# Optimization experiments

Hardware: AMD Instinct MI355X
Metric: run time of the kernel (lower is better)

Reference implementation:

```python
import jax, jax.numpy as jnp
import numpy as np

N_NODES = 100000
N_EDGES = 1600000
D_IN = 128
D_OUT = 128


def setup_inputs() -> dict:
    key = jax.random.key(0)
    k1, k2, k3, k4, k5 = jax.random.split(key, 5)
    x = jax.random.normal(k1, (N_NODES, D_IN), dtype=jnp.float32)
    row = jax.random.randint(k2, (N_EDGES,), 0, N_NODES, dtype=jnp.int32)
    col = jax.random.randint(k3, (N_EDGES,), 0, N_NODES, dtype=jnp.int32)
    edge_weight = jax.random.uniform(k4, (N_EDGES,), dtype=jnp.float32)
    stdv = 1.0 / np.sqrt(D_OUT)
    weight = jax.random.uniform(k5, (D_IN, D_OUT), dtype=jnp.float32,
                                minval=-stdv, maxval=stdv)
    return {"x": x, "row": row, "col": col,
            "edge_weight": edge_weight, "weight": weight}


def reference(x, row, col, edge_weight, weight):
    # support = x @ W  -- dense feature transform [N, D_OUT]
    support = jnp.matmul(x, weight)
    # out = adj @ support, adj sparse COO: out[row] += w * support[col]
    messages = edge_weight[:, None] * support[col]  # [E, D_OUT]
    out = jax.ops.segment_sum(messages, row, num_segments=N_NODES)
    return out
```

## Files before the change

kernel.cpp:

```cpp
#include <hip/hip_runtime.h>

#define N_NODES 100000
#define N_EDGES 1600000
#define D 128
#define D4 32

#define BM 128
#define GEMM_BLOCKS ((N_NODES + BM - 1) / BM)
#define BUILD_BLOCKS 512
#define TOTAL_BLOCKS (BUILD_BLOCKS + GEMM_BLOCKS)
#define LDK 136

typedef __attribute__((ext_vector_type(8))) short short8;
typedef __attribute__((ext_vector_type(4))) float floatx4;

__device__ __forceinline__ unsigned short f2bf(float f) {
    unsigned int b = __float_as_uint(f);
    b += 0x7FFFu + ((b >> 16) & 1u);
    return (unsigned short)(b >> 16);
}
__device__ __forceinline__ float bf2f(unsigned short u) {
    return __uint_as_float((unsigned int)u << 16);
}

__global__ __launch_bounds__(256) void w_prep(
    const float* __restrict__ W, unsigned short* __restrict__ wt)
{
    int idx = blockIdx.x * 256 + threadIdx.x;
    int k = idx >> 7, n = idx & 127;
    wt[(size_t)n * D + k] = f2bf(W[idx]);
}

__global__ __launch_bounds__(256, 4) void mega(
    const float* __restrict__ x, const unsigned short* __restrict__ wt,
    unsigned short* __restrict__ sup,
    const int* __restrict__ row, const int* __restrict__ col,
    const float* __restrict__ ew,
    int* __restrict__ head, int4* __restrict__ entries)
{
    __shared__ unsigned short xs[BM * LDK];

    const int tid = threadIdx.x;

    if (blockIdx.x < BUILD_BLOCKS) {
        const int S = BUILD_BLOCKS * 256;
        const int par = tid & 1;
        for (int e = blockIdx.x * 256 + tid; e < N_EDGES; e += S) {
            int nx = atomicExch(&head[(row[e] << 1) | par], e);
            entries[e] = make_int4(nx, col[e], __float_as_int(ew[e]), 0);
        }
        return;
    }

    const int brow = (blockIdx.x - BUILD_BLOCKS) * BM;

    {
        const float4* xv = reinterpret_cast<const float4*>(x);
        #pragma unroll
        for (int i = 0; i < 16; ++i) {
            int idx = tid + i * 256;
            int r = idx >> 5, k4 = idx & 31;
            int gr = brow + r;
            float4 v = (gr < N_NODES) ? xv[(size_t)gr * D4 + k4]
                                      : make_float4(0.f, 0.f, 0.f, 0.f);
            ushort4 p;
            p.x = f2bf(v.x); p.y = f2bf(v.y); p.z = f2bf(v.z); p.w = f2bf(v.w);
            *reinterpret_cast<ushort4*>(&xs[r * LDK + k4 * 4]) = p;
        }
    }
    __syncthreads();

    const int wave = tid >> 6;
    const int lane = tid & 63;
    const int l15  = lane & 15;
    const int lkg  = lane >> 4;

    floatx4 acc[2][8];
    #pragma unroll
    for (int m = 0; m < 2; ++m)
        #pragma unroll
        for (int n = 0; n < 8; ++n) acc[m][n] = (floatx4){0.f, 0.f, 0.f, 0.f};

    const short8* bv = reinterpret_cast<const short8*>(wt);
    const int wrow = wave * 32;
    #pragma unroll
    for (int kk = 0; kk < 4; ++kk) {
        int kb = kk * 32 + lkg * 8;
        short8 a0 = *reinterpret_cast<const short8*>(&xs[(wrow + l15) * LDK + kb]);
        short8 a1 = *reinterpret_cast<const short8*>(&xs[(wrow + 16 + l15) * LDK + kb]);
        #pragma unroll
        for (int n = 0; n < 8; ++n) {
            short8 b = bv[(n * 16 + l15) * 16 + kk * 4 + lkg];
            acc[0][n] = __builtin_amdgcn_mfma_f32_16x16x32_bf16(a0, b, acc[0][n], 0, 0, 0);
            acc[1][n] = __builtin_amdgcn_mfma_f32_16x16x32_bf16(a1, b, acc[1][n], 0, 0, 0);
        }
    }

    const int rbase = brow + wrow + lkg * 4;
    #pragma unroll
    for (int m = 0; m < 2; ++m) {
        #pragma unroll
        for (int r = 0; r < 4; ++r) {
            int grow = rbase + m * 16 + r;
            if (grow < N_NODES) {
                #pragma unroll
                for (int n = 0; n < 8; ++n)
                    sup[(size_t)grow * D + n * 16 + l15] = f2bf(acc[m][n][r]);
            }
        }
    }
}

#define GATHER_BLOCKS (N_NODES / 16)

__global__ __launch_bounds__(256) void gather_list(
    const int* __restrict__ head, const int4* __restrict__ entries,
    const unsigned short* __restrict__ sup, float* __restrict__ out)
{
    const int half = threadIdx.x >> 5;
    const int lane = threadIdx.x & 31;
    const int nb = blockIdx.x * 16 + half * 2;

    int4 h = *reinterpret_cast<const int4*>(head + 2 * nb);
    int e0 = h.x, e1 = h.y, e2 = h.z, e3 = h.w;

    float4 A0 = {0.f, 0.f, 0.f, 0.f};
    float4 A1 = A0, A2 = A0, A3 = A0;

    while (e0 >= 0 || e1 >= 0 || e2 >= 0 || e3 >= 0) {
        int4 q0 = entries[e0 >= 0 ? e0 : 0];
        int4 q1 = entries[e1 >= 0 ? e1 : 0];
        int4 q2 = entries[e2 >= 0 ? e2 : 0];
        int4 q3 = entries[e3 >= 0 ? e3 : 0];

        ushort4 s0 = reinterpret_cast<const ushort4*>(sup + (size_t)q0.y * D)[lane];
        ushort4 s1 = reinterpret_cast<const ushort4*>(sup + (size_t)q1.y * D)[lane];
        ushort4 s2 = reinterpret_cast<const ushort4*>(sup + (size_t)q2.y * D)[lane];
        ushort4 s3 = reinterpret_cast<const ushort4*>(sup + (size_t)q3.y * D)[lane];

        float w0 = (e0 >= 0) ? __int_as_float(q0.z) : 0.f;
        float w1 = (e1 >= 0) ? __int_as_float(q1.z) : 0.f;
        float w2 = (e2 >= 0) ? __int_as_float(q2.z) : 0.f;
        float w3 = (e3 >= 0) ? __int_as_float(q3.z) : 0.f;

        A0.x = fmaf(w0, bf2f(s0.x), A0.x); A0.y = fmaf(w0, bf2f(s0.y), A0.y);
        A0.z = fmaf(w0, bf2f(s0.z), A0.z); A0.w = fmaf(w0, bf2f(s0.w), A0.w);
        A1.x = fmaf(w1, bf2f(s1.x), A1.x); A1.y = fmaf(w1, bf2f(s1.y), A1.y);
        A1.z = fmaf(w1, bf2f(s1.z), A1.z); A1.w = fmaf(w1, bf2f(s1.w), A1.w);
        A2.x = fmaf(w2, bf2f(s2.x), A2.x); A2.y = fmaf(w2, bf2f(s2.y), A2.y);
        A2.z = fmaf(w2, bf2f(s2.z), A2.z); A2.w = fmaf(w2, bf2f(s2.w), A2.w);
        A3.x = fmaf(w3, bf2f(s3.x), A3.x); A3.y = fmaf(w3, bf2f(s3.y), A3.y);
        A3.z = fmaf(w3, bf2f(s3.z), A3.z); A3.w = fmaf(w3, bf2f(s3.w), A3.w);

        e0 = (e0 >= 0) ? q0.x : -1;
        e1 = (e1 >= 0) ? q1.x : -1;
        e2 = (e2 >= 0) ? q2.x : -1;
        e3 = (e3 >= 0) ? q3.x : -1;
    }

    float4 a0, a1;
    a0.x = A0.x + A1.x; a0.y = A0.y + A1.y; a0.z = A0.z + A1.z; a0.w = A0.w + A1.w;
    a1.x = A2.x + A3.x; a1.y = A2.y + A3.y; a1.z = A2.z + A3.z; a1.w = A2.w + A3.w;

    float4* ov = reinterpret_cast<float4*>(out);
    ov[(size_t)(nb + 0) * D4 + lane] = a0;
    ov[(size_t)(nb + 1) * D4 + lane] = a1;
}

__device__ __forceinline__ void fma4(float4& a, float s, const float4& b) {
    a.x = fmaf(s, b.x, a.x);
    a.y = fmaf(s, b.y, a.y);
    a.z = fmaf(s, b.z, a.z);
    a.w = fmaf(s, b.w, a.w);
}

__global__ __launch_bounds__(256) void gemm_xw(
    const float* __restrict__ x, const float* __restrict__ W,
    unsigned short* __restrict__ sup)
{
    __shared__ float4 xs[32 * D4];
    const int tid = threadIdx.x;
    const int block_row = blockIdx.x * 32;

    const float4* xv = reinterpret_cast<const float4*>(x) + (size_t)block_row * D4;
    #pragma unroll
    for (int i = 0; i < 4; ++i) xs[tid + i * 256] = xv[tid + i * 256];
    __syncthreads();

    const int cg = tid & 31;
    const int rg = tid >> 5;
    const float4* Wv = reinterpret_cast<const float4*>(W);

    float4 acc0 = {0.f, 0.f, 0.f, 0.f};
    float4 acc1 = acc0, acc2 = acc0, acc3 = acc0;

    const int r0 = rg * 4;
    #pragma unroll 8
    for (int k4 = 0; k4 < D4; ++k4) {
        float4 xa = xs[(r0 + 0) * D4 + k4];
        float4 xb = xs[(r0 + 1) * D4 + k4];
        float4 xc = xs[(r0 + 2) * D4 + k4];
        float4 xd = xs[(r0 + 3) * D4 + k4];
        float4 w0 = Wv[(k4 * 4 + 0) * D4 + cg];
        fma4(acc0, xa.x, w0); fma4(acc1, xb.x, w0);
        fma4(acc2, xc.x, w0); fma4(acc3, xd.x, w0);
        float4 w1 = Wv[(k4 * 4 + 1) * D4 + cg];
        fma4(acc0, xa.y, w1); fma4(acc1, xb.y, w1);
        fma4(acc2, xc.y, w1); fma4(acc3, xd.y, w1);
        float4 w2 = Wv[(k4 * 4 + 2) * D4 + cg];
        fma4(acc0, xa.z, w2); fma4(acc1, xb.z, w2);
        fma4(acc2, xc.z, w2); fma4(acc3, xd.z, w2);
        float4 w3 = Wv[(k4 * 4 + 3) * D4 + cg];
        fma4(acc0, xa.w, w3); fma4(acc1, xb.w, w3);
        fma4(acc2, xc.w, w3); fma4(acc3, xd.w, w3);
    }

    ushort4 p;
    #define STORE_BF16(ACC, R)                                            \
        p.x = f2bf(ACC.x); p.y = f2bf(ACC.y);                             \
        p.z = f2bf(ACC.z); p.w = f2bf(ACC.w);                             \
        *reinterpret_cast<ushort4*>(sup + (size_t)(block_row + r0 + R) * D + cg * 4) = p;
    STORE_BF16(acc0, 0)
    STORE_BF16(acc1, 1)
    STORE_BF16(acc2, 2)
    STORE_BF16(acc3, 3)
    #undef STORE_BF16
}

__global__ __launch_bounds__(256) void scatter_edges(
    const int* __restrict__ row, const int* __restrict__ col,
    const float* __restrict__ ew, const unsigned short* __restrict__ sup,
    float* __restrict__ out)
{
    const int e = blockIdx.x * 8 + (threadIdx.x >> 5);
    if (e >= N_EDGES) return;
    const int lane = threadIdx.x & 31;

    const int r = row[e];
    const int c = col[e];
    const float w = ew[e];
    ushort4 s = reinterpret_cast<const ushort4*>(sup + (size_t)c * D)[lane];
    float* o = out + (size_t)r * D + lane * 4;
    atomicAdd(o + 0, w * bf2f(s.x));
    atomicAdd(o + 1, w * bf2f(s.y));
    atomicAdd(o + 2, w * bf2f(s.z));
    atomicAdd(o + 3, w * bf2f(s.w));
}

extern "C" void kernel_launch(void* const* d_in, const int* in_sizes, int n_in,
                              void* d_out, int out_size, void* d_ws, size_t ws_size,
                              hipStream_t stream)
{
    const float* x      = (const float*)d_in[0];
    const int*   row    = (const int*)d_in[1];
    const int*   col    = (const int*)d_in[2];
    const float* ew     = (const float*)d_in[3];
    const float* weight = (const float*)d_in[4];
    float* out = (float*)d_out;

    char* ws = (char*)d_ws;
    const size_t off_sup     = 0;
    const size_t off_head    = off_sup + (size_t)N_NODES * D * 2;
    const size_t off_entries = off_head + (((size_t)N_NODES * 8 + 15) & ~(size_t)15);
    const size_t off_wt      = off_entries + (size_t)N_EDGES * 16;
    const size_t required    = off_wt + (size_t)D * D * 2;

    unsigned short* sup = (unsigned short*)(ws + off_sup);

    if (ws_size >= required) {
        int*  head    = (int*)(ws + off_head);
        int4* entries = (int4*)(ws + off_entries);
        unsigned short* wt = (unsigned short*)(ws + off_wt);

        hipMemsetAsync(head, 0xFF, (size_t)N_NODES * 8, stream);
        w_prep<<<D * D / 256, 256, 0, stream>>>(weight, wt);

        mega<<<TOTAL_BLOCKS, 256, 0, stream>>>(
            x, wt, sup, row, col, ew, head, entries);

        gather_list<<<GATHER_BLOCKS, 256, 0, stream>>>(head, entries, sup, out);
    } else {
        gemm_xw<<<N_NODES / 32, 256, 0, stream>>>(x, weight, sup);
        hipMemsetAsync(d_out, 0, (size_t)N_NODES * D * sizeof(float), stream);
        scatter_edges<<<N_EDGES / 8, 256, 0, stream>>>(row, col, ew, sup, out);
    }
}
```

Measured before the change: 186.0 us.

## Fold head memset into prep kernel and use dynamic node refill in gather

The separate memset of the head array is merged into the weight-prep kernel, which removes one launch. The gather kernel changes from a fixed assignment of two nodes per half-wave to a per-block shared counter, so each half-wave pulls new nodes as soon as its current linked lists end. This aims to reduce load imbalance from uneven in-degree across nodes. The cost is shared-memory atomics, extra control flow and divergence in the loop, plus fewer independent edge chains in flight per half-wave.

Result: slower. 191.5 us (+2.9%).

```diff
diff --git a/kernel.cpp b/kernel.cpp
--- a/kernel.cpp
+++ b/kernel.cpp
@@ -11,6 +11,9 @@
 #define TOTAL_BLOCKS (BUILD_BLOCKS + GEMM_BLOCKS)
 #define LDK 136
 
+#define G_NODES 32
+#define GATHER_BLOCKS (N_NODES / G_NODES)
+
 typedef __attribute__((ext_vector_type(8))) short short8;
 typedef __attribute__((ext_vector_type(4))) float floatx4;
 
@@ -23,12 +26,23 @@
     return __uint_as_float((unsigned int)u << 16);
 }
 
-__global__ __launch_bounds__(256) void w_prep(
-    const float* __restrict__ W, unsigned short* __restrict__ wt)
-{
-    int idx = blockIdx.x * 256 + threadIdx.x;
-    int k = idx >> 7, n = idx & 127;
-    wt[(size_t)n * D + k] = f2bf(W[idx]);
+#define PREP_WT_BLOCKS 64
+#define PREP_HEAD_BLOCKS ((N_NODES * 2 / 4 + 255) / 256)
+#define PREP_BLOCKS (PREP_WT_BLOCKS + PREP_HEAD_BLOCKS)
+
+__global__ __launch_bounds__(256) void prep(
+    const float* __restrict__ W, unsigned short* __restrict__ wt,
+    int* __restrict__ head)
+{
+    if (blockIdx.x < PREP_WT_BLOCKS) {
+        int idx = blockIdx.x * 256 + threadIdx.x;
+        int k = idx >> 7, n = idx & 127;
+        wt[(size_t)n * D + k] = f2bf(W[idx]);
+    } else {
+        int i = ((blockIdx.x - PREP_WT_BLOCKS) * 256 + threadIdx.x) * 4;
+        if (i < N_NODES * 2)
+            *reinterpret_cast<int4*>(head + i) = make_int4(-1, -1, -1, -1);
+    }
 }
 
 __global__ __launch_bounds__(256, 4) void mega(
@@ -111,60 +125,90 @@
     }
 }
 
-#define GATHER_BLOCKS (N_NODES / 16)
-
-__global__ __launch_bounds__(256) void gather_list(
+__global__ __launch_bounds__(256) void gather_refill(
     const int* __restrict__ head, const int4* __restrict__ entries,
     const unsigned short* __restrict__ sup, float* __restrict__ out)
 {
-    const int half = threadIdx.x >> 5;
-    const int lane = threadIdx.x & 31;
-    const int nb = blockIdx.x * 16 + half * 2;
-
-    int4 h = *reinterpret_cast<const int4*>(head + 2 * nb);
-    int e0 = h.x, e1 = h.y, e2 = h.z, e3 = h.w;
-
-    float4 A0 = {0.f, 0.f, 0.f, 0.f};
-    float4 A1 = A0, A2 = A0, A3 = A0;
-
-    while (e0 >= 0 || e1 >= 0 || e2 >= 0 || e3 >= 0) {
-        int4 q0 = entries[e0 >= 0 ? e0 : 0];
-        int4 q1 = entries[e1 >= 0 ? e1 : 0];
-        int4 q2 = entries[e2 >= 0 ? e2 : 0];
-        int4 q3 = entries[e3 >= 0 ? e3 : 0];
-
-        ushort4 s0 = reinterpret_cast<const ushort4*>(sup + (size_t)q0.y * D)[lane];
-        ushort4 s1 = reinterpret_cast<const ushort4*>(sup + (size_t)q1.y * D)[lane];
-        ushort4 s2 = reinterpret_cast<const ushort4*>(sup + (size_t)q2.y * D)[lane];
-        ushort4 s3 = reinterpret_cast<const ushort4*>(sup + (size_t)q3.y * D)[lane];
-
-        float w0 = (e0 >= 0) ? __int_as_float(q0.z) : 0.f;
-        float w1 = (e1 >= 0) ? __int_as_float(q1.z) : 0.f;
-        float w2 = (e2 >= 0) ? __int_as_float(q2.z) : 0.f;
-        float w3 = (e3 >= 0) ? __int_as_float(q3.z) : 0.f;
-
-        A0.x = fmaf(w0, bf2f(s0.x), A0.x); A0.y = fmaf(w0, bf2f(s0.y), A0.y);
-        A0.z = fmaf(w0, bf2f(s0.z), A0.z); A0.w = fmaf(w0, bf2f(s0.w), A0.w);
-        A1.x = fmaf(w1, bf2f(s1.x), A1.x); A1.y = fmaf(w1, bf2f(s1.y), A1.y);
-        A1.z = fmaf(w1, bf2f(s1.z), A1.z); A1.w = fmaf(w1, bf2f(s1.w), A1.w);
-        A2.x = fmaf(w2, bf2f(s2.x), A2.x); A2.y = fmaf(w2, bf2f(s2.y), A2.y);
-        A2.z = fmaf(w2, bf2f(s2.z), A2.z); A2.w = fmaf(w2, bf2f(s2.w), A2.w);
-        A3.x = fmaf(w3, bf2f(s3.x), A3.x); A3.y = fmaf(w3, bf2f(s3.y), A3.y);
-        A3.z = fmaf(w3, bf2f(s3.z), A3.z); A3.w = fmaf(w3, bf2f(s3.w), A3.w);
-
-        e0 = (e0 >= 0) ? q0.x : -1;
-        e1 = (e1 >= 0) ? q1.x : -1;
-        e2 = (e2 >= 0) ? q2.x : -1;
-        e3 = (e3 >= 0) ? q3.x : -1;
-    }
-
-    float4 a0, a1;
-    a0.x = A0.x + A1.x; a0.y = A0.y + A1.y; a0.z = A0.z + A1.z; a0.w = A0.w + A1.w;
-    a1.x = A2.x + A3.x; a1.y = A2.y + A3.y; a1.z = A2.z + A3.z; a1.w = A2.w + A3.w;
-
+    __shared__ int ctr;
+    const int tid = threadIdx.x;
+    if (tid == 0) ctr = 0;
+    __syncthreads();
+
+    const int lane = tid & 31;
+    const int src0 = tid & 32;
+    const int base = blockIdx.x * G_NODES;
+    const ushort4* supv = reinterpret_cast<const ushort4*>(sup);
     float4* ov = reinterpret_cast<float4*>(out);
-    ov[(size_t)(nb + 0) * D4 + lane] = a0;
-    ov[(size_t)(nb + 1) * D4 + lane] = a1;
+
+    int nodeA = -1, eA0 = -1, eA1 = -1;
+    int nodeB = -1, eB0 = -1, eB1 = -1;
+    float4 accA = {0.f, 0.f, 0.f, 0.f};
+    float4 accB = accA;
+    bool more = true;
+
+    while (true) {
+        if (nodeA < 0 && more) {
+            int t = 0;
+            if (lane == 0) t = atomicAdd(&ctr, 1);
+            int idx = __shfl(t, src0, 64);
+            if (idx < G_NODES) {
+                nodeA = base + idx;
+                int2 h = *reinterpret_cast<const int2*>(head + 2 * nodeA);
+                eA0 = h.x; eA1 = h.y;
+                accA = make_float4(0.f, 0.f, 0.f, 0.f);
+            } else more = false;
+        }
+        if (nodeB < 0 && more) {
+            int t = 0;
+            if (lane == 0) t = atomicAdd(&ctr, 1);
+            int idx = __shfl(t, src0, 64);
+            if (idx < G_NODES) {
+                nodeB = base + idx;
+                int2 h = *reinterpret_cast<const int2*>(head + 2 * nodeB);
+                eB0 = h.x; eB1 = h.y;
+                accB = make_float4(0.f, 0.f, 0.f, 0.f);
+            } else more = false;
+        }
+        if (nodeA < 0 && nodeB < 0) break;
+
+        int4 qa0 = entries[eA0 >= 0 ? eA0 : 0];
+        int4 qa1 = entries[eA1 >= 0 ? eA1 : 0];
+        int4 qb0 = entries[eB0 >= 0 ? eB0 : 0];
+        int4 qb1 = entries[eB1 >= 0 ? eB1 : 0];
+
+        ushort4 sa0 = supv[(size_t)qa0.y * D4 + lane];
+        ushort4 sa1 = supv[(size_t)qa1.y * D4 + lane];
+        ushort4 sb0 = supv[(size_t)qb0.y * D4 + lane];
+        ushort4 sb1 = supv[(size_t)qb1.y * D4 + lane];
+
+        float wa0 = (eA0 >= 0) ? __int_as_float(qa0.z) : 0.f;
+        float wa1 = (eA1 >= 0) ? __int_as_float(qa1.z) : 0.f;
+        float wb0 = (eB0 >= 0) ? __int_as_float(qb0.z) : 0.f;
+        float wb1 = (eB1 >= 0) ? __int_as_float(qb1.z) : 0.f;
+
+        accA.x = fmaf(wa0, bf2f(sa0.x), accA.x); accA.x = fmaf(wa1, bf2f(sa1.x), accA.x);
+        accA.y = fmaf(wa0, bf2f(sa0.y), accA.y); accA.y = fmaf(wa1, bf2f(sa1.y), accA.y);
+        accA.z = fmaf(wa0, bf2f(sa0.z), accA.z); accA.z = fmaf(wa1, bf2f(sa1.z), accA.z);
+        accA.w = fmaf(wa0, bf2f(sa0.w), accA.w); accA.w = fmaf(wa1, bf2f(sa1.w), accA.w);
+        accB.x = fmaf(wb0, bf2f(sb0.x), accB.x); accB.x = fmaf(wb1, bf2f(sb1.x), accB.x);
+        accB.y = fmaf(wb0, bf2f(sb0.y), accB.y); accB.y = fmaf(wb1, bf2f(sb1.y), accB.y);
+        accB.z = fmaf(wb0, bf2f(sb0.z), accB.z); accB.z = fmaf(wb1, bf2f(sb1.z), accB.z);
+        accB.w = fmaf(wb0, bf2f(sb0.w), accB.w); accB.w = fmaf(wb1, bf2f(sb1.w), accB.w);
+
+        eA0 = (eA0 >= 0) ? qa0.x : -1;
+        eA1 = (eA1 >= 0) ? qa1.x : -1;
+        eB0 = (eB0 >= 0) ? qb0.x : -1;
+        eB1 = (eB1 >= 0) ? qb1.x : -1;
+
+        if (nodeA >= 0 && eA0 < 0 && eA1 < 0) {
+            ov[(size_t)nodeA * D4 + lane] = accA;
+            nodeA = -1;
+        }
+        if (nodeB >= 0 && eB0 < 0 && eB1 < 0) {
+            ov[(size_t)nodeB * D4 + lane] = accB;
+            nodeB = -1;
+        }
+    }
 }
 
 __device__ __forceinline__ void fma4(float4& a, float s, const float4& b) {
@@ -272,13 +316,12 @@
         int4* entries = (int4*)(ws + off_entries);
         unsigned short* wt = (unsigned short*)(ws + off_wt);
 
-        hipMemsetAsync(head, 0xFF, (size_t)N_NODES * 8, stream);
-        w_prep<<<D * D / 256, 256, 0, stream>>>(weight, wt);
+        prep<<<PREP_BLOCKS, 256, 0, stream>>>(weight, wt, head);
 
         mega<<<TOTAL_BLOCKS, 256, 0, stream>>>(
             x, wt, sup, row, col, ew, head, entries);
 
-        gather_list<<<GATHER_BLOCKS, 256, 0, stream>>>(head, entries, sup, out);
+        gather_refill<<<GATHER_BLOCKS, 256, 0, stream>>>(head, entries, sup, out);
     } else {
         gemm_xw<<<N_NODES / 32, 256, 0, stream>>>(x, weight, sup);
         hipMemsetAsync(d_out, 0, (size_t)N_NODES * D * sizeof(float), stream);
```

## Fuse head memset into prep kernel and halve GEMM tile for occupancy

Applied to the files above, without the earlier changes.

Replaces the hipMemsetAsync of the head array and the separate W transpose kernel with one prep kernel that does both, removing a launch. The GEMM part of the mega kernel now uses 64-row tiles with a 2x2 wave layout (32 rows by 64 columns per wave). This halves LDS use and accumulator registers, so launch bounds can ask for 8 blocks per CU. The cost is twice as many GEMM blocks, and each block reads the full weight matrix again.

New measurement: 177.4 us. -4.6%, faster.

```diff
diff --git a/kernel.cpp b/kernel.cpp
--- a/kernel.cpp
+++ b/kernel.cpp
@@ -5,12 +5,14 @@
 #define D 128
 #define D4 32
 
-#define BM 128
+#define BM 64
 #define GEMM_BLOCKS ((N_NODES + BM - 1) / BM)
 #define BUILD_BLOCKS 512
 #define TOTAL_BLOCKS (BUILD_BLOCKS + GEMM_BLOCKS)
 #define LDK 136
 
+#define GATHER_BLOCKS (N_NODES / 16)
+
 typedef __attribute__((ext_vector_type(8))) short short8;
 typedef __attribute__((ext_vector_type(4))) float floatx4;
 
@@ -23,15 +25,26 @@
     return __uint_as_float((unsigned int)u << 16);
 }
 
-__global__ __launch_bounds__(256) void w_prep(
-    const float* __restrict__ W, unsigned short* __restrict__ wt)
-{
-    int idx = blockIdx.x * 256 + threadIdx.x;
-    int k = idx >> 7, n = idx & 127;
-    wt[(size_t)n * D + k] = f2bf(W[idx]);
-}
-
-__global__ __launch_bounds__(256, 4) void mega(
+#define PREP_WT_BLOCKS 64
+#define PREP_HEAD_BLOCKS ((N_NODES * 2 / 4 + 255) / 256)
+#define PREP_BLOCKS (PREP_WT_BLOCKS + PREP_HEAD_BLOCKS)
+
+__global__ __launch_bounds__(256) void prep(
+    const float* __restrict__ W, unsigned short* __restrict__ wt,
+    int* __restrict__ head)
+{
+    if (blockIdx.x < PREP_WT_BLOCKS) {
+        int idx = blockIdx.x * 256 + threadIdx.x;
+        int k = idx >> 7, n = idx & 127;
+        wt[(size_t)n * D + k] = f2bf(W[idx]);
+    } else {
+        int i = ((blockIdx.x - PREP_WT_BLOCKS) * 256 + threadIdx.x) * 4;
+        if (i < N_NODES * 2)
+            *reinterpret_cast<int4*>(head + i) = make_int4(-1, -1, -1, -1);
+    }
+}
+
+__global__ __launch_bounds__(256, 8) void mega(
     const float* __restrict__ x, const unsigned short* __restrict__ wt,
     unsigned short* __restrict__ sup,
     const int* __restrict__ row, const int* __restrict__ col,
@@ -57,7 +70,7 @@
     {
         const float4* xv = reinterpret_cast<const float4*>(x);
         #pragma unroll
-        for (int i = 0; i < 16; ++i) {
+        for (int i = 0; i < 8; ++i) {
             int idx = tid + i * 256;
             int r = idx >> 5, k4 = idx & 31;
             int gr = brow + r;
@@ -74,29 +87,30 @@
     const int lane = tid & 63;
     const int l15  = lane & 15;
     const int lkg  = lane >> 4;
-
-    floatx4 acc[2][8];
+    const int wr   = (wave & 1) * 32;
+    const int wc   = (wave >> 1) * 64;
+
+    floatx4 acc[2][4];
     #pragma unroll
     for (int m = 0; m < 2; ++m)
         #pragma unroll
-        for (int n = 0; n < 8; ++n) acc[m][n] = (floatx4){0.f, 0.f, 0.f, 0.f};
+        for (int n = 0; n < 4; ++n) acc[m][n] = (floatx4){0.f, 0.f, 0.f, 0.f};
 
     const short8* bv = reinterpret_cast<const short8*>(wt);
-    const int wrow = wave * 32;
     #pragma unroll
     for (int kk = 0; kk < 4; ++kk) {
         int kb = kk * 32 + lkg * 8;
-        short8 a0 = *reinterpret_cast<const short8*>(&xs[(wrow + l15) * LDK + kb]);
-        short8 a1 = *reinterpret_cast<const short8*>(&xs[(wrow + 16 + l15) * LDK + kb]);
-        #pragma unroll
-        for (int n = 0; n < 8; ++n) {
-            short8 b = bv[(n * 16 + l15) * 16 + kk * 4 + lkg];
+        short8 a0 = *reinterpret_cast<const short8*>(&xs[(wr + l15) * LDK + kb]);
+        short8 a1 = *reinterpret_cast<const short8*>(&xs[(wr + 16 + l15) * LDK + kb]);
+        #pragma unroll
+        for (int n = 0; n < 4; ++n) {
+            short8 b = bv[(wc + n * 16 + l15) * 16 + kk * 4 + lkg];
             acc[0][n] = __builtin_amdgcn_mfma_f32_16x16x32_bf16(a0, b, acc[0][n], 0, 0, 0);
             acc[1][n] = __builtin_amdgcn_mfma_f32_16x16x32_bf16(a1, b, acc[1][n], 0, 0, 0);
         }
     }
 
-    const int rbase = brow + wrow + lkg * 4;
+    const int rbase = brow + wr + lkg * 4;
     #pragma unroll
     for (int m = 0; m < 2; ++m) {
         #pragma unroll
@@ -104,14 +118,12 @@
             int grow = rbase + m * 16 + r;
             if (grow < N_NODES) {
                 #pragma unroll
-                for (int n = 0; n < 8; ++n)
-                    sup[(size_t)grow * D + n * 16 + l15] = f2bf(acc[m][n][r]);
+                for (int n = 0; n < 4; ++n)
+                    sup[(size_t)grow * D + wc + n * 16 + l15] = f2bf(acc[m][n][r]);
             }
         }
     }
 }
-
-#define GATHER_BLOCKS (N_NODES / 16)
 
 __global__ __launch_bounds__(256) void gather_list(
     const int* __restrict__ head, const int4* __restrict__ entries,
@@ -272,8 +284,7 @@
         int4* entries = (int4*)(ws + off_entries);
         unsigned short* wt = (unsigned short*)(ws + off_wt);
 
-        hipMemsetAsync(head, 0xFF, (size_t)N_NODES * 8, stream);
-        w_prep<<<D * D / 256, 256, 0, stream>>>(weight, wt);
+        prep<<<PREP_BLOCKS, 256, 0, stream>>>(weight, wt, head);
 
         mega<<<TOTAL_BLOCKS, 256, 0, stream>>>(
             x, wt, sup, row, col, ew, head, entries);
```
